# Performance work log

Measured on AMD Instinct MI355X. Metric: run time of the kernel, lower is better.

Reference implementation:

```python
import jax, jax.numpy as jnp
import numpy as np

N_NODES = 100000
N_EDGES = 1600000
F_IN, HID, N_CLS = 64, 64, 40
K = 3  # Chebyshev order


def setup_inputs() -> dict:
    key = jax.random.key(0)
    k = jax.random.split(key, 7)
    x = jax.random.normal(k[0], (N_NODES, F_IN), dtype=jnp.float32)
    edge_index = jax.random.randint(k[1], (2, N_EDGES), 0, N_NODES, dtype=jnp.int32)
    W1 = jax.random.normal(k[2], (K, F_IN, HID), dtype=jnp.float32) * 0.05
    b1 = jax.random.normal(k[3], (HID,), dtype=jnp.float32) * 0.05
    W2 = jax.random.normal(k[4], (K, HID, N_CLS), dtype=jnp.float32) * 0.05
    b2 = jax.random.normal(k[5], (N_CLS,), dtype=jnp.float32) * 0.05
    return {"x": x, "edge_index": edge_index, "W1": W1, "b1": b1, "W2": W2, "b2": b2}


def _norm(edge_index, n):
    # PyG ChebConv with sym normalization and lambda_max=2.0:
    # L_hat edge weight = -deg^{-1/2}[src] * deg^{-1/2}[dst]; self-loop weight 0.
    src, dst = edge_index[0], edge_index[1]
    keep = (src != dst).astype(jnp.float32)  # remove_self_loops
    deg = jax.ops.segment_sum(keep, src, num_segments=n)
    dis = jnp.where(deg > 0, 1.0 / jnp.sqrt(jnp.maximum(deg, 1.0)), 0.0)
    w = -dis[src] * dis[dst] * keep
    return src, dst, w


def _spmm(x, src, dst, w, n):
    # out[i] = sum_{e: dst[e]==i} w[e] * x[src[e]]
    return jax.ops.segment_sum(w[:, None] * x[src], dst, num_segments=n)


def _cheb_conv(x, src, dst, w, W, b, n):
    Tx0 = x
    out = Tx0 @ W[0]
    Tx1 = _spmm(x, src, dst, w, n)
    out = out + Tx1 @ W[1]
    for k in range(2, W.shape[0]):
        Tx2 = 2.0 * _spmm(Tx1, src, dst, w, n) - Tx0
        out = out + Tx2 @ W[k]
        Tx0, Tx1 = Tx1, Tx2
    return out + b


def reference(x, edge_index, W1, b1, W2, b2):
    n = x.shape[0]
    src, dst, w = _norm(edge_index, n)
    h = jax.nn.relu(_cheb_conv(x, src, dst, w, W1, b1, n))
    out = _cheb_conv(h, src, dst, w, W2, b2, n)
    return jax.nn.softmax(out, axis=1)
```

## Files before the change

kernel.cpp:

```cpp
#include <hip/hip_runtime.h>

#define N_NODES 100000
#define N_EDGES 1600000
#define NCLS 40
#define NBUCK 196
#define CAPE 8960
#define CAPC 10752
#define DUMMY N_NODES

typedef unsigned short u16;
typedef unsigned int u32;
typedef short bf16x8 __attribute__((ext_vector_type(8)));
typedef float f32x4 __attribute__((ext_vector_type(4)));

static inline size_t align256(size_t x) { return (x + 255) & ~(size_t)255; }

__device__ __forceinline__ float bf2f(u16 h) { return __uint_as_float(((u32)h) << 16); }
__device__ __forceinline__ u16 f2bf(float f) {
    u32 u = __float_as_uint(f);
    u += 0x7FFFu + ((u >> 16) & 1u);
    return (u16)(u >> 16);
}
__device__ __forceinline__ u32 pk2(u16 a, u16 b) { return (u32)a | ((u32)b << 16); }

#define PS_BLOCKS 391
#define CONV_BLOCKS 6250

__global__ __launch_bounds__(256) void pscatter_conv(const int* __restrict__ src,
                                                     const int* __restrict__ dst,
                                                     int* __restrict__ gFillD,
                                                     int* __restrict__ gFillS,
                                                     int2* __restrict__ partD,
                                                     int* __restrict__ partS,
                                                     const float* __restrict__ x,
                                                     u16* __restrict__ xb) {
    if (blockIdx.x >= PS_BLOCKS) {
        int i = (blockIdx.x - PS_BLOCKS) * 256 + threadIdx.x;
        float4 v = *(const float4*)(x + (size_t)i * 4);
        ushort4 o;
        o.x = f2bf(v.x); o.y = f2bf(v.y); o.z = f2bf(v.z); o.w = f2bf(v.w);
        *(ushort4*)(xb + (size_t)i * 4) = o;
        return;
    }
    __shared__ int histD[NBUCK], histS[NBUCK], chunkD[NBUCK], chunkS[NBUCK];
    int tid = threadIdx.x;
    int base = blockIdx.x * 4096;

    int4 sv[4], dv[4];
#pragma unroll
    for (int j = 0; j < 4; ++j) {
        int idx = base + j * 1024 + tid * 4;
        if (idx < N_EDGES) {
            sv[j] = *(const int4*)(src + idx);
            dv[j] = *(const int4*)(dst + idx);
        } else {
            sv[j] = make_int4(0, 0, 0, 0);
            dv[j] = make_int4(0, 0, 0, 0);
        }
    }

    for (int i = tid; i < NBUCK; i += 256) { histD[i] = 0; histS[i] = 0; }
    __syncthreads();
#pragma unroll
    for (int j = 0; j < 4; ++j)
#pragma unroll
        for (int k = 0; k < 4; ++k) {
            int s = ((const int*)&sv[j])[k], d = ((const int*)&dv[j])[k];
            if (s != d) {
                atomicAdd(&histD[d >> 9], 1);
                atomicAdd(&histS[s >> 9], 1);
            }
        }
    __syncthreads();
    for (int B = tid; B < NBUCK; B += 256) {
        int cD = histD[B];
        chunkD[B] = cD ? atomicAdd(&gFillD[B], cD) : 0;
        int cS = histS[B];
        chunkS[B] = cS ? atomicAdd(&gFillS[B], cS) : 0;
    }
    __syncthreads();
    for (int i = tid; i < NBUCK; i += 256) { histD[i] = 0; histS[i] = 0; }
    __syncthreads();
#pragma unroll
    for (int j = 0; j < 4; ++j)
#pragma unroll
        for (int k = 0; k < 4; ++k) {
            int s = ((const int*)&sv[j])[k], d = ((const int*)&dv[j])[k];
            if (s != d) {
                int bD = d >> 9;
                int r = atomicAdd(&histD[bD], 1);
                int o = chunkD[bD] + r;
                if (o < CAPE) partD[bD * CAPE + o] = make_int2(d, s);
                int bS = s >> 9;
                int r2 = atomicAdd(&histS[bS], 1);
                int o2 = chunkS[bS] + r2;
                if (o2 < CAPE) partS[bS * CAPE + o2] = s;
            }
        }
}

__global__ __launch_bounds__(256) void build(const int2* __restrict__ partD,
                                             const int* __restrict__ partS,
                                             const int* __restrict__ gFillD,
                                             const int* __restrict__ gFillS,
                                             int* __restrict__ csr,
                                             int2* __restrict__ meta,
                                             float* __restrict__ dis) {
    __shared__ int cnt[512], loc[512], rnk[512];
    int tid = threadIdx.x;

    if (blockIdx.x >= NBUCK) {
        int B = blockIdx.x - NBUCK;
        for (int i = tid; i < 512; i += 256) cnt[i] = 0;
        __syncthreads();
        int nS = min(gFillS[B], CAPE);
        for (int i = tid; i < nS; i += 256) atomicAdd(&cnt[partS[B * CAPE + i] & 511], 1);
        __syncthreads();
        for (int n = tid; n < 512; n += 256) {
            int node = B * 512 + n;
            if (node < N_NODES) {
                int dg = cnt[n];
                dis[node] = dg > 0 ? 1.0f / sqrtf((float)dg) : 0.0f;
            }
        }
        return;
    }

    int B = blockIdx.x;
    for (int i = tid; i < 512; i += 256) { cnt[i] = 0; rnk[i] = 0; }
    __syncthreads();
    int nD = min(gFillD[B], CAPE);
    for (int i = tid; i < nD; i += 256) atomicAdd(&cnt[partD[B * CAPE + i].x & 511], 1);
    __syncthreads();
    if (tid < 64) {
        int bb = tid * 8, c8[8], mysum = 0;
#pragma unroll
        for (int j = 0; j < 8; ++j) { c8[j] = (cnt[bb + j] + 7) & ~7; mysum += c8[j]; }
        int incl = mysum;
#pragma unroll
        for (int off = 1; off < 64; off <<= 1) {
            int v = __shfl_up(incl, off);
            if (tid >= off) incl += v;
        }
        int run = incl - mysum;
#pragma unroll
        for (int j = 0; j < 8; ++j) { loc[bb + j] = run; run += c8[j]; }
    }
    __syncthreads();
    for (int n = tid; n < 512; n += 256) {
        int node = B * 512 + n;
        if (node < N_NODES) {
            meta[node] = make_int2(B * CAPC + loc[n], cnt[n]);
            int c = cnt[n], c8 = (c + 7) & ~7;
            for (int e = c; e < c8; ++e) csr[B * CAPC + loc[n] + e] = DUMMY;
        }
    }
    for (int i = tid; i < nD; i += 256) {
        int2 p = partD[B * CAPE + i];
        int ln = p.x & 511;
        int r = atomicAdd(&rnk[ln], 1);
        int pos = loc[ln] + r;
        if (pos < CAPC) csr[B * CAPC + pos] = p.y;
    }
}

__global__ __launch_bounds__(256) void spmm(const u16* __restrict__ in,
                                            const float* __restrict__ dis,
                                            const int2* __restrict__ meta,
                                            const int* __restrict__ csr,
                                            u16* __restrict__ outhi,
                                            u16* __restrict__ outlo) {
    int node = (blockIdx.x * 256 + threadIdx.x) >> 6;
    int lane = threadIdx.x & 63;
    if (node >= N_NODES) return;
    int2 mt = meta[node];
    int c8 = (mt.y + 7) & ~7;
    const int* lst = csr + mt.x;
    const u32* in32 = (const u32*)in;
    const int hsel = lane >> 5;
    const int fl = lane & 31;
    float acc0 = 0.0f, acc1 = 0.0f;
    int e = 0;
    for (; e + 16 <= c8; e += 16) {
        int4 sa = *(const int4*)(lst + e);
        int4 sb = *(const int4*)(lst + e + 4);
        int4 sc = *(const int4*)(lst + e + 8);
        int4 sd = *(const int4*)(lst + e + 12);
        int s0 = hsel ? sa.y : sa.x;
        int s1 = hsel ? sa.w : sa.z;
        int s2 = hsel ? sb.y : sb.x;
        int s3 = hsel ? sb.w : sb.z;
        int s4 = hsel ? sc.y : sc.x;
        int s5 = hsel ? sc.w : sc.z;
        int s6 = hsel ? sd.y : sd.x;
        int s7 = hsel ? sd.w : sd.z;
        u32 v0 = in32[((u32)s0 << 5) + fl];
        u32 v1 = in32[((u32)s1 << 5) + fl];
        u32 v2 = in32[((u32)s2 << 5) + fl];
        u32 v3 = in32[((u32)s3 << 5) + fl];
        u32 v4 = in32[((u32)s4 << 5) + fl];
        u32 v5 = in32[((u32)s5 << 5) + fl];
        u32 v6 = in32[((u32)s6 << 5) + fl];
        u32 v7 = in32[((u32)s7 << 5) + fl];
        float w0 = dis[s0], w1 = dis[s1], w2 = dis[s2], w3 = dis[s3];
        float w4 = dis[s4], w5 = dis[s5], w6 = dis[s6], w7 = dis[s7];
        acc0 = fmaf(w0, __uint_as_float(v0 << 16), acc0);
        acc1 = fmaf(w0, __uint_as_float(v0 & 0xFFFF0000u), acc1);
        acc0 = fmaf(w1, __uint_as_float(v1 << 16), acc0);
        acc1 = fmaf(w1, __uint_as_float(v1 & 0xFFFF0000u), acc1);
        acc0 = fmaf(w2, __uint_as_float(v2 << 16), acc0);
        acc1 = fmaf(w2, __uint_as_float(v2 & 0xFFFF0000u), acc1);
        acc0 = fmaf(w3, __uint_as_float(v3 << 16), acc0);
        acc1 = fmaf(w3, __uint_as_float(v3 & 0xFFFF0000u), acc1);
        acc0 = fmaf(w4, __uint_as_float(v4 << 16), acc0);
        acc1 = fmaf(w4, __uint_as_float(v4 & 0xFFFF0000u), acc1);
        acc0 = fmaf(w5, __uint_as_float(v5 << 16), acc0);
        acc1 = fmaf(w5, __uint_as_float(v5 & 0xFFFF0000u), acc1);
        acc0 = fmaf(w6, __uint_as_float(v6 << 16), acc0);
        acc1 = fmaf(w6, __uint_as_float(v6 & 0xFFFF0000u), acc1);
        acc0 = fmaf(w7, __uint_as_float(v7 << 16), acc0);
        acc1 = fmaf(w7, __uint_as_float(v7 & 0xFFFF0000u), acc1);
    }
    if (e < c8) {
        int4 sa = *(const int4*)(lst + e);
        int4 sb = *(const int4*)(lst + e + 4);
        int s0 = hsel ? sa.y : sa.x;
        int s1 = hsel ? sa.w : sa.z;
        int s2 = hsel ? sb.y : sb.x;
        int s3 = hsel ? sb.w : sb.z;
        u32 v0 = in32[((u32)s0 << 5) + fl];
        u32 v1 = in32[((u32)s1 << 5) + fl];
        u32 v2 = in32[((u32)s2 << 5) + fl];
        u32 v3 = in32[((u32)s3 << 5) + fl];
        float w0 = dis[s0], w1 = dis[s1], w2 = dis[s2], w3 = dis[s3];
        acc0 = fmaf(w0, __uint_as_float(v0 << 16), acc0);
        acc1 = fmaf(w0, __uint_as_float(v0 & 0xFFFF0000u), acc1);
        acc0 = fmaf(w1, __uint_as_float(v1 << 16), acc0);
        acc1 = fmaf(w1, __uint_as_float(v1 & 0xFFFF0000u), acc1);
        acc0 = fmaf(w2, __uint_as_float(v2 << 16), acc0);
        acc1 = fmaf(w2, __uint_as_float(v2 & 0xFFFF0000u), acc1);
        acc0 = fmaf(w3, __uint_as_float(v3 << 16), acc0);
        acc1 = fmaf(w3, __uint_as_float(v3 & 0xFFFF0000u), acc1);
    }
    acc0 += __shfl_xor(acc0, 32);
    acc1 += __shfl_xor(acc1, 32);
    float vd = -dis[node];
    float f0 = vd * acc0, f1 = vd * acc1;
    u32 o32 = ((u32)node << 5) + fl;
    u16 h0 = f2bf(f0), h1 = f2bf(f1);
    if (hsel == 0) {
        ((u32*)outhi)[o32] = pk2(h0, h1);
    } else {
        ((u32*)outlo)[o32] = pk2(f2bf(f0 - bf2f(h0)), f2bf(f1 - bf2f(h1)));
    }
}

#define DGRID 1250
#define DNT 5
#define LSTR 200

__device__ __forceinline__ float foldW(const float* __restrict__ W, int kk, int col,
                                       int ncols) {
    float wv = W[kk * ncols + col];
    if (kk < 64) wv -= W[(kk + 128) * ncols + col];
    else if (kk >= 128) wv += wv;
    return wv;
}

__global__ __launch_bounds__(256) void dense1_mf(const float* __restrict__ x,
                                                 const u16* __restrict__ a1h,
                                                 const u16* __restrict__ a1l,
                                                 const u16* __restrict__ tyh,
                                                 const u16* __restrict__ tyl,
                                                 const float* __restrict__ W,
                                                 const float* __restrict__ bias,
                                                 u16* __restrict__ ohi,
                                                 u16* __restrict__ olo) {
    __shared__ u16 Ah[16 * LSTR], Al[16 * LSTR];
    const int tid = threadIdx.x, wid = tid >> 6, lane = tid & 63;
    const int lrow = lane & 15, lk8 = (lane >> 4) * 8;
    const int col = wid * 16 + lrow;

    bf16x8 wh[6], wl[6];
#pragma unroll
    for (int c = 0; c < 6; ++c) {
        bf16x8 h, l;
#pragma unroll
        for (int i = 0; i < 8; ++i) {
            float wv = foldW(W, c * 32 + lk8 + i, col, 64);
            u16 hb_ = f2bf(wv);
            h[i] = (short)hb_;
            l[i] = (short)f2bf(wv - bf2f(hb_));
        }
        wh[c] = h; wl[c] = l;
    }
    float bv = bias[col];
    const int srow = tid >> 4, sc4 = (tid & 15) * 4;

    for (int t = 0; t < DNT; ++t) {
        int r0 = (blockIdx.x * DNT + t) * 16;
        size_t rb = ((size_t)(r0 + srow) << 6) + sc4;
        {
            float4 v = *(const float4*)&x[rb];
            const float* vp = (const float*)&v;
            ushort4 hv, lv;
#pragma unroll
            for (int i = 0; i < 4; ++i) {
                u16 hb_ = f2bf(vp[i]);
                ((u16*)&hv)[i] = hb_;
                ((u16*)&lv)[i] = f2bf(vp[i] - bf2f(hb_));
            }
            *(ushort4*)&Ah[srow * LSTR + sc4] = hv;
            *(ushort4*)&Al[srow * LSTR + sc4] = lv;
        }
        *(ushort4*)&Ah[srow * LSTR + 64 + sc4] = *(const ushort4*)&a1h[rb];
        *(ushort4*)&Al[srow * LSTR + 64 + sc4] = *(const ushort4*)&a1l[rb];
        *(ushort4*)&Ah[srow * LSTR + 128 + sc4] = *(const ushort4*)&tyh[rb];
        *(ushort4*)&Al[srow * LSTR + 128 + sc4] = *(const ushort4*)&tyl[rb];
        __syncthreads();

        f32x4 acc = {bv, bv, bv, bv};
#pragma unroll
        for (int c = 0; c < 6; ++c) {
            bf16x8 ah = *(const bf16x8*)&Ah[lrow * LSTR + c * 32 + lk8];
            bf16x8 al = *(const bf16x8*)&Al[lrow * LSTR + c * 32 + lk8];
            acc = __builtin_amdgcn_mfma_f32_16x16x32_bf16(ah, wh[c], acc, 0, 0, 0);
            acc = __builtin_amdgcn_mfma_f32_16x16x32_bf16(al, wh[c], acc, 0, 0, 0);
            acc = __builtin_amdgcn_mfma_f32_16x16x32_bf16(ah, wl[c], acc, 0, 0, 0);
        }
        __syncthreads();

#pragma unroll
        for (int j = 0; j < 4; ++j) {
            int row = r0 + (lane >> 4) * 4 + j;
            float v = fmaxf(acc[j], 0.0f);
            u16 hb_ = f2bf(v);
            ohi[((size_t)row << 6) + col] = hb_;
            olo[((size_t)row << 6) + col] = f2bf(v - bf2f(hb_));
        }
    }
}

__global__ __launch_bounds__(256) void dense2_mf(const u16* __restrict__ a0h,
                                                 const u16* __restrict__ a0l,
                                                 const u16* __restrict__ a1h,
                                                 const u16* __restrict__ a1l,
                                                 const u16* __restrict__ tyh,
                                                 const u16* __restrict__ tyl,
                                                 const float* __restrict__ W,
                                                 const float* __restrict__ bias,
                                                 float* __restrict__ out) {
    __shared__ u16 Ah[16 * LSTR], Al[16 * LSTR];
    __shared__ float Ls[16][48];
    const int tid = threadIdx.x, wid = tid >> 6, lane = tid & 63;
    const int lrow = lane & 15, lk8 = (lane >> 4) * 8;
    const int col = wid * 16 + lrow;
    const bool act = (wid < 3);
    const bool cok = act && (col < NCLS);

    bf16x8 wh[6], wl[6];
#pragma unroll
    for (int c = 0; c < 6; ++c) {
        bf16x8 h = 0, l = 0;
        if (cok) {
#pragma unroll
            for (int i = 0; i < 8; ++i) {
                float wv = foldW(W, c * 32 + lk8 + i, col, NCLS);
                u16 hb_ = f2bf(wv);
                h[i] = (short)hb_;
                l[i] = (short)f2bf(wv - bf2f(hb_));
            }
        }
        wh[c] = h; wl[c] = l;
    }
    float bv = cok ? bias[col] : 0.0f;
    const int srow = tid >> 4, sc4 = (tid & 15) * 4;

    for (int t = 0; t < DNT; ++t) {
        int r0 = (blockIdx.x * DNT + t) * 16;
        size_t rb = ((size_t)(r0 + srow) << 6) + sc4;
        *(ushort4*)&Ah[srow * LSTR + sc4] = *(const ushort4*)&a0h[rb];
        *(ushort4*)&Al[srow * LSTR + sc4] = *(const ushort4*)&a0l[rb];
        *(ushort4*)&Ah[srow * LSTR + 64 + sc4] = *(const ushort4*)&a1h[rb];
        *(ushort4*)&Al[srow * LSTR + 64 + sc4] = *(const ushort4*)&a1l[rb];
        *(ushort4*)&Ah[srow * LSTR + 128 + sc4] = *(const ushort4*)&tyh[rb];
        *(ushort4*)&Al[srow * LSTR + 128 + sc4] = *(const ushort4*)&tyl[rb];
        __syncthreads();

        if (act) {
            f32x4 acc = {bv, bv, bv, bv};
#pragma unroll
            for (int c = 0; c < 6; ++c) {
                bf16x8 ah = *(const bf16x8*)&Ah[lrow * LSTR + c * 32 + lk8];
                bf16x8 al = *(const bf16x8*)&Al[lrow * LSTR + c * 32 + lk8];
                acc = __builtin_amdgcn_mfma_f32_16x16x32_bf16(ah, wh[c], acc, 0, 0, 0);
                acc = __builtin_amdgcn_mfma_f32_16x16x32_bf16(al, wh[c], acc, 0, 0, 0);
                acc = __builtin_amdgcn_mfma_f32_16x16x32_bf16(ah, wl[c], acc, 0, 0, 0);
            }
#pragma unroll
            for (int j = 0; j < 4; ++j) Ls[(lane >> 4) * 4 + j][col] = acc[j];
        }
        __syncthreads();

        {
            int row = wid * 4 + (lane >> 4);
            int cg = lane & 15;
            float v0 = Ls[row][cg];
            float v1 = Ls[row][cg + 16];
            float v2 = (cg < 8) ? Ls[row][cg + 32] : -1e30f;
            float m = fmaxf(fmaxf(v0, v1), v2);
#pragma unroll
            for (int o = 8; o; o >>= 1) m = fmaxf(m, __shfl_xor(m, o));
            float e0 = expf(v0 - m), e1 = expf(v1 - m);
            float e2 = (cg < 8) ? expf(v2 - m) : 0.0f;
            float s = e0 + e1 + e2;
#pragma unroll
            for (int o = 8; o; o >>= 1) s += __shfl_xor(s, o);
            float inv = 1.0f / s;
            size_t ob = (size_t)(r0 + row) * NCLS;
            out[ob + cg] = e0 * inv;
            out[ob + cg + 16] = e1 * inv;
            if (cg < 8) out[ob + cg + 32] = e2 * inv;
        }
    }
}


extern "C" void kernel_launch(void* const* d_in, const int* in_sizes, int n_in,
                              void* d_out, int out_size, void* d_ws, size_t ws_size,
                              hipStream_t stream) {
    const float* x = (const float*)d_in[0];
    const int* edge_index = (const int*)d_in[1];
    const float* W1 = (const float*)d_in[2];
    const float* b1 = (const float*)d_in[3];
    const float* W2 = (const float*)d_in[4];
    const float* b2 = (const float*)d_in[5];
    float* out = (float*)d_out;

    const int* src = edge_index;
    const int* dst = edge_index + N_EDGES;

    char* ws = (char*)d_ws;
    size_t off = 0;
    auto carve = [&](size_t bytes) -> void* {
        void* p = ws + off;
        off = align256(off + bytes);
        return p;
    };
    int* gFillD = (int*)carve((size_t)NBUCK * 4);
    int* gFillS = (int*)carve((size_t)NBUCK * 4);
    size_t zero_bytes = off;
    int2* partD = (int2*)carve((size_t)NBUCK * CAPE * 8);
    int* partS = (int*)carve((size_t)NBUCK * CAPE * 4);
    int* csr = (int*)carve((size_t)NBUCK * CAPC * 4 + 1024);
    int2* meta = (int2*)carve((size_t)N_NODES * 8);
    float* dis = (float*)carve((size_t)(N_NODES + 1) * 4);
    const size_t FB = (size_t)(N_NODES + 1) * 64 * 2;
    u16* xb  = (u16*)carve(FB);
    u16* t1h = (u16*)carve(FB);
    u16* t1l = (u16*)carve(FB);
    u16* tyh = (u16*)carve(FB);
    u16* tyl = (u16*)carve(FB);
    u16* hh  = (u16*)carve(FB);
    u16* hl  = (u16*)carve(FB);

    const int WV = (N_NODES * 64) / 256;

    hipMemsetAsync(d_ws, 0, zero_bytes, stream);
    hipMemsetAsync(dis + N_NODES, 0, 4, stream);
    hipMemsetAsync(xb + (size_t)N_NODES * 64, 0, 128, stream);
    hipMemsetAsync(t1h + (size_t)N_NODES * 64, 0, 128, stream);
    hipMemsetAsync(hh + (size_t)N_NODES * 64, 0, 128, stream);

    pscatter_conv<<<PS_BLOCKS + CONV_BLOCKS, 256, 0, stream>>>(src, dst, gFillD, gFillS,
                                                               partD, partS, x, xb);
    build<<<2 * NBUCK, 256, 0, stream>>>(partD, partS, gFillD, gFillS, csr, meta, dis);

    spmm<<<WV, 256, 0, stream>>>(xb, dis, meta, csr, t1h, t1l);
    spmm<<<WV, 256, 0, stream>>>(t1h, dis, meta, csr, tyh, tyl);
    dense1_mf<<<DGRID, 256, 0, stream>>>(x, t1h, t1l, tyh, tyl, W1, b1, hh, hl);

    spmm<<<WV, 256, 0, stream>>>(hh, dis, meta, csr, t1h, t1l);
    spmm<<<WV, 256, 0, stream>>>(t1h, dis, meta, csr, tyh, tyl);
    dense2_mf<<<DGRID, 256, 0, stream>>>(hh, hl, t1h, t1l, tyh, tyl, W2, b2, out);
}
```

Baseline: 270.7 us.

## Pack source index and fp16 weight into CSR entries, split build kernel

```diff
diff --git a/kernel.cpp b/kernel.cpp
--- a/kernel.cpp
+++ b/kernel.cpp
@@ -1,4 +1,5 @@
 #include <hip/hip_runtime.h>
+#include <hip/hip_fp16.h>
 
 #define N_NODES 100000
 #define N_EDGES 1600000
@@ -22,6 +23,12 @@
     return (u16)(u >> 16);
 }
 __device__ __forceinline__ u32 pk2(u16 a, u16 b) { return (u32)a | ((u32)b << 16); }
+__device__ __forceinline__ u32 pack15(float f) {
+    return ((u32)__half_as_ushort(__float2half(f))) & 0x7FFFu;
+}
+__device__ __forceinline__ float unpack15(u32 bits) {
+    return __half2float(__ushort_as_half((u16)bits));
+}
 
 #define PS_BLOCKS 391
 #define CONV_BLOCKS 6250
@@ -30,7 +37,7 @@
                                                      const int* __restrict__ dst,
                                                      int* __restrict__ gFillD,
                                                      int* __restrict__ gFillS,
-                                                     int2* __restrict__ partD,
+                                                     u32* __restrict__ partD,
                                                      int* __restrict__ partS,
                                                      const float* __restrict__ x,
                                                      u16* __restrict__ xb) {
@@ -90,7 +97,7 @@
                 int bD = d >> 9;
                 int r = atomicAdd(&histD[bD], 1);
                 int o = chunkD[bD] + r;
-                if (o < CAPE) partD[bD * CAPE + o] = make_int2(d, s);
+                if (o < CAPE) partD[bD * CAPE + o] = ((u32)s << 9) | (u32)(d & 511);
                 int bS = s >> 9;
                 int r2 = atomicAdd(&histS[bS], 1);
                 int o2 = chunkS[bS] + r2;
@@ -99,38 +106,38 @@
         }
 }
 
-__global__ __launch_bounds__(256) void build(const int2* __restrict__ partD,
-                                             const int* __restrict__ partS,
-                                             const int* __restrict__ gFillD,
-                                             const int* __restrict__ gFillS,
-                                             int* __restrict__ csr,
-                                             int2* __restrict__ meta,
-                                             float* __restrict__ dis) {
+__global__ __launch_bounds__(256) void build_dis(const int* __restrict__ partS,
+                                                 const int* __restrict__ gFillS,
+                                                 float* __restrict__ dis) {
+    __shared__ int cnt[512];
+    int tid = threadIdx.x;
+    int B = blockIdx.x;
+    for (int i = tid; i < 512; i += 256) cnt[i] = 0;
+    __syncthreads();
+    int nS = min(gFillS[B], CAPE);
+    for (int i = tid; i < nS; i += 256) atomicAdd(&cnt[partS[B * CAPE + i] & 511], 1);
+    __syncthreads();
+    for (int n = tid; n < 512; n += 256) {
+        int node = B * 512 + n;
+        if (node < N_NODES) {
+            int dg = cnt[n];
+            dis[node] = dg > 0 ? 1.0f / sqrtf((float)dg) : 0.0f;
+        }
+    }
+}
+
+__global__ __launch_bounds__(256) void build_csr(const u32* __restrict__ partD,
+                                                 const int* __restrict__ gFillD,
+                                                 const float* __restrict__ dis,
+                                                 u32* __restrict__ csr,
+                                                 int2* __restrict__ meta) {
     __shared__ int cnt[512], loc[512], rnk[512];
     int tid = threadIdx.x;
-
-    if (blockIdx.x >= NBUCK) {
-        int B = blockIdx.x - NBUCK;
-        for (int i = tid; i < 512; i += 256) cnt[i] = 0;
-        __syncthreads();
-        int nS = min(gFillS[B], CAPE);
-        for (int i = tid; i < nS; i += 256) atomicAdd(&cnt[partS[B * CAPE + i] & 511], 1);
-        __syncthreads();
-        for (int n = tid; n < 512; n += 256) {
-            int node = B * 512 + n;
-            if (node < N_NODES) {
-                int dg = cnt[n];
-                dis[node] = dg > 0 ? 1.0f / sqrtf((float)dg) : 0.0f;
-            }
-        }
-        return;
-    }
-
     int B = blockIdx.x;
     for (int i = tid; i < 512; i += 256) { cnt[i] = 0; rnk[i] = 0; }
     __syncthreads();
     int nD = min(gFillD[B], CAPE);
-    for (int i = tid; i < nD; i += 256) atomicAdd(&cnt[partD[B * CAPE + i].x & 511], 1);
+    for (int i = tid; i < nD; i += 256) atomicAdd(&cnt[partD[B * CAPE + i] & 511], 1);
     __syncthreads();
     if (tid < 64) {
         int bb = tid * 8, c8[8], mysum = 0;
@@ -152,22 +159,23 @@
         if (node < N_NODES) {
             meta[node] = make_int2(B * CAPC + loc[n], cnt[n]);
             int c = cnt[n], c8 = (c + 7) & ~7;
-            for (int e = c; e < c8; ++e) csr[B * CAPC + loc[n] + e] = DUMMY;
+            for (int e = c; e < c8; ++e) csr[B * CAPC + loc[n] + e] = (u32)DUMMY;
         }
     }
     for (int i = tid; i < nD; i += 256) {
-        int2 p = partD[B * CAPE + i];
-        int ln = p.x & 511;
+        u32 p = partD[B * CAPE + i];
+        int ln = p & 511;
+        u32 s = p >> 9;
         int r = atomicAdd(&rnk[ln], 1);
         int pos = loc[ln] + r;
-        if (pos < CAPC) csr[B * CAPC + pos] = p.y;
+        if (pos < CAPC) csr[B * CAPC + pos] = s | (pack15(dis[s]) << 17);
     }
 }
 
 __global__ __launch_bounds__(256) void spmm(const u16* __restrict__ in,
                                             const float* __restrict__ dis,
                                             const int2* __restrict__ meta,
-                                            const int* __restrict__ csr,
+                                            const u32* __restrict__ csr,
                                             u16* __restrict__ outhi,
                                             u16* __restrict__ outlo) {
     int node = (blockIdx.x * 256 + threadIdx.x) >> 6;
@@ -175,35 +183,37 @@
     if (node >= N_NODES) return;
     int2 mt = meta[node];
     int c8 = (mt.y + 7) & ~7;
-    const int* lst = csr + mt.x;
+    const u32* lst = csr + mt.x;
     const u32* in32 = (const u32*)in;
     const int hsel = lane >> 5;
     const int fl = lane & 31;
     float acc0 = 0.0f, acc1 = 0.0f;
     int e = 0;
     for (; e + 16 <= c8; e += 16) {
-        int4 sa = *(const int4*)(lst + e);
-        int4 sb = *(const int4*)(lst + e + 4);
-        int4 sc = *(const int4*)(lst + e + 8);
-        int4 sd = *(const int4*)(lst + e + 12);
-        int s0 = hsel ? sa.y : sa.x;
-        int s1 = hsel ? sa.w : sa.z;
-        int s2 = hsel ? sb.y : sb.x;
-        int s3 = hsel ? sb.w : sb.z;
-        int s4 = hsel ? sc.y : sc.x;
-        int s5 = hsel ? sc.w : sc.z;
-        int s6 = hsel ? sd.y : sd.x;
-        int s7 = hsel ? sd.w : sd.z;
-        u32 v0 = in32[((u32)s0 << 5) + fl];
-        u32 v1 = in32[((u32)s1 << 5) + fl];
-        u32 v2 = in32[((u32)s2 << 5) + fl];
-        u32 v3 = in32[((u32)s3 << 5) + fl];
-        u32 v4 = in32[((u32)s4 << 5) + fl];
-        u32 v5 = in32[((u32)s5 << 5) + fl];
-        u32 v6 = in32[((u32)s6 << 5) + fl];
-        u32 v7 = in32[((u32)s7 << 5) + fl];
-        float w0 = dis[s0], w1 = dis[s1], w2 = dis[s2], w3 = dis[s3];
-        float w4 = dis[s4], w5 = dis[s5], w6 = dis[s6], w7 = dis[s7];
+        uint4 ea = *(const uint4*)(lst + e);
+        uint4 eb = *(const uint4*)(lst + e + 4);
+        uint4 ec = *(const uint4*)(lst + e + 8);
+        uint4 ed = *(const uint4*)(lst + e + 12);
+        u32 e0 = hsel ? ea.y : ea.x;
+        u32 e1 = hsel ? ea.w : ea.z;
+        u32 e2 = hsel ? eb.y : eb.x;
+        u32 e3 = hsel ? eb.w : eb.z;
+        u32 e4 = hsel ? ec.y : ec.x;
+        u32 e5 = hsel ? ec.w : ec.z;
+        u32 e6 = hsel ? ed.y : ed.x;
+        u32 e7 = hsel ? ed.w : ed.z;
+        u32 v0 = in32[((e0 & 0x1FFFFu) << 5) + fl];
+        u32 v1 = in32[((e1 & 0x1FFFFu) << 5) + fl];
+        u32 v2 = in32[((e2 & 0x1FFFFu) << 5) + fl];
+        u32 v3 = in32[((e3 & 0x1FFFFu) << 5) + fl];
+        u32 v4 = in32[((e4 & 0x1FFFFu) << 5) + fl];
+        u32 v5 = in32[((e5 & 0x1FFFFu) << 5) + fl];
+        u32 v6 = in32[((e6 & 0x1FFFFu) << 5) + fl];
+        u32 v7 = in32[((e7 & 0x1FFFFu) << 5) + fl];
+        float w0 = unpack15(e0 >> 17), w1 = unpack15(e1 >> 17);
+        float w2 = unpack15(e2 >> 17), w3 = unpack15(e3 >> 17);
+        float w4 = unpack15(e4 >> 17), w5 = unpack15(e5 >> 17);
+        float w6 = unpack15(e6 >> 17), w7 = unpack15(e7 >> 17);
         acc0 = fmaf(w0, __uint_as_float(v0 << 16), acc0);
         acc1 = fmaf(w0, __uint_as_float(v0 & 0xFFFF0000u), acc1);
         acc0 = fmaf(w1, __uint_as_float(v1 << 16), acc0);
@@ -222,17 +232,18 @@
         acc1 = fmaf(w7, __uint_as_float(v7 & 0xFFFF0000u), acc1);
     }
     if (e < c8) {
-        int4 sa = *(const int4*)(lst + e);
-        int4 sb = *(const int4*)(lst + e + 4);
-        int s0 = hsel ? sa.y : sa.x;
-        int s1 = hsel ? sa.w : sa.z;
-        int s2 = hsel ? sb.y : sb.x;
-        int s3 = hsel ? sb.w : sb.z;
-        u32 v0 = in32[((u32)s0 << 5) + fl];
-        u32 v1 = in32[((u32)s1 << 5) + fl];
-        u32 v2 = in32[((u32)s2 << 5) + fl];
-        u32 v3 = in32[((u32)s3 << 5) + fl];
-        float w0 = dis[s0], w1 = dis[s1], w2 = dis[s2], w3 = dis[s3];
+        uint4 ea = *(const uint4*)(lst + e);
+        uint4 eb = *(const uint4*)(lst + e + 4);
+        u32 e0 = hsel ? ea.y : ea.x;
+        u32 e1 = hsel ? ea.w : ea.z;
+        u32 e2 = hsel ? eb.y : eb.x;
+        u32 e3 = hsel ? eb.w : eb.z;
+        u32 v0 = in32[((e0 & 0x1FFFFu) << 5) + fl];
+        u32 v1 = in32[((e1 & 0x1FFFFu) << 5) + fl];
+        u32 v2 = in32[((e2 & 0x1FFFFu) << 5) + fl];
+        u32 v3 = in32[((e3 & 0x1FFFFu) << 5) + fl];
+        float w0 = unpack15(e0 >> 17), w1 = unpack15(e1 >> 17);
+        float w2 = unpack15(e2 >> 17), w3 = unpack15(e3 >> 17);
         acc0 = fmaf(w0, __uint_as_float(v0 << 16), acc0);
         acc1 = fmaf(w0, __uint_as_float(v0 & 0xFFFF0000u), acc1);
         acc0 = fmaf(w1, __uint_as_float(v1 << 16), acc0);
@@ -255,8 +266,8 @@
     }
 }
 
-#define DGRID 1250
-#define DNT 5
+#define DGRID 625
+#define DNT 10
 #define LSTR 200
 
 __device__ __forceinline__ float foldW(const float* __restrict__ W, int kk, int col,
@@ -450,9 +461,9 @@
     int* gFillD = (int*)carve((size_t)NBUCK * 4);
     int* gFillS = (int*)carve((size_t)NBUCK * 4);
     size_t zero_bytes = off;
-    int2* partD = (int2*)carve((size_t)NBUCK * CAPE * 8);
+    u32* partD = (u32*)carve((size_t)NBUCK * CAPE * 4);
     int* partS = (int*)carve((size_t)NBUCK * CAPE * 4);
-    int* csr = (int*)carve((size_t)NBUCK * CAPC * 4 + 1024);
+    u32* csr = (u32*)carve((size_t)NBUCK * CAPC * 4 + 1024);
     int2* meta = (int2*)carve((size_t)N_NODES * 8);
     float* dis = (float*)carve((size_t)(N_NODES + 1) * 4);
     const size_t FB = (size_t)(N_NODES + 1) * 64 * 2;
@@ -474,7 +485,8 @@
 
     pscatter_conv<<<PS_BLOCKS + CONV_BLOCKS, 256, 0, stream>>>(src, dst, gFillD, gFillS,
                                                                partD, partS, x, xb);
-    build<<<2 * NBUCK, 256, 0, stream>>>(partD, partS, gFillD, gFillS, csr, meta, dis);
+    build_dis<<<NBUCK, 256, 0, stream>>>(partS, gFillS, dis);
+    build_csr<<<NBUCK, 256, 0, stream>>>(partD, gFillD, dis, csr, meta);
 
     spmm<<<WV, 256, 0, stream>>>(xb, dis, meta, csr, t1h, t1l);
     spmm<<<WV, 256, 0, stream>>>(t1h, dis, meta, csr, tyh, tyl);
```

Result: slower. 276.7 us (+2.2%).
